# Kernel optimization log

Measured on AMD Instinct MI355X. Metric: run time of the kernel, lower is better.

## Reference

```python
import jax, jax.numpy as jnp
import numpy as np

BATCH, SEQ, IN_DIM, HID = 32, 4096, 256, 256

def setup_inputs() -> dict:
    key = jax.random.key(0)
    ks = jax.random.split(key, 7)
    s_in = 1.0 / np.sqrt(IN_DIM)
    s_h = 1.0 / np.sqrt(HID)
    return {
        "X": jax.random.normal(ks[0], (BATCH, SEQ, IN_DIM), dtype=jnp.float32),
        "Wx_w": jax.random.uniform(ks[1], (HID, IN_DIM), jnp.float32, -s_in, s_in),
        "Wx_b": jax.random.uniform(ks[2], (HID,), jnp.float32, -s_in, s_in),
        "Wh_w": jax.random.uniform(ks[3], (HID, HID), jnp.float32, -s_h, s_h),
        "Wh_b": jax.random.uniform(ks[4], (HID,), jnp.float32, -s_h, s_h),
        "Wy_w": jax.random.uniform(ks[5], (HID, HID), jnp.float32, -s_h, s_h),
        "Wy_b": jax.random.uniform(ks[6], (HID,), jnp.float32, -s_h, s_h),
    }

def reference(X, Wx_w, Wx_b, Wh_w, Wh_b, Wy_w, Wy_b):
    # X: [B, T, D] -> time-major [T, B, D]
    Xt = jnp.transpose(X, (1, 0, 2))
    B = X.shape[0]
    h0 = jnp.zeros((B, Wh_w.shape[0]), dtype=X.dtype)
    # Precompute input projection for all timesteps in one big GEMM
    Xproj = jnp.einsum('tbd,hd->tbh', Xt, Wx_w) + Wx_b  # [T, B, H]

    def step(h, xp):
        h = jnp.tanh(h @ Wh_w.T + Wh_b + xp)   # [B, H]
        y = h @ Wy_w.T + Wy_b                   # [B, H]
        return h, y

    _, Ys = jax.lax.scan(step, h0, Xproj)       # Ys: [T, B, H]
    # torch.cat along dim 0 of per-step [B, H] tensors -> [T*B, H]
    return Ys.reshape(-1, Ys.shape[-1])
```

## Files before the change

kernel.cpp:

```cpp
#include <hip/hip_runtime.h>
#include <cmath>

#define TSEQ 4096
#define NB   32
#define DIM  256

__global__ __launch_bounds__(256) void k1_xproj(
    const float* __restrict__ X, const float* __restrict__ Wx,
    const float* __restrict__ bx, const float* __restrict__ bh,
    float* __restrict__ out)
{
    __shared__ __align__(16) float As[32][68];
    __shared__ __align__(16) float Bs[32][68];
    const int tid = threadIdx.x;
    const int r0 = blockIdx.x * 64;
    const int n0 = blockIdx.y * 64;
    const int tm = tid >> 4, tn = tid & 15;
    const int lr = tid >> 2;
    const int lk = (tid & 3) * 8;

    const int rg = r0 + lr;
    const float* arow = X + ((size_t)(rg & 31) * TSEQ + (size_t)(rg >> 5)) * DIM;
    const float* brow = Wx + (size_t)(n0 + lr) * DIM;

    float acc[4][4] = {};

    for (int k0 = 0; k0 < DIM; k0 += 32) {
        float4 a0 = *(const float4*)(arow + k0 + lk);
        float4 a1 = *(const float4*)(arow + k0 + lk + 4);
        float4 b0 = *(const float4*)(brow + k0 + lk);
        float4 b1 = *(const float4*)(brow + k0 + lk + 4);
        __syncthreads();
        As[lk+0][lr]=a0.x; As[lk+1][lr]=a0.y; As[lk+2][lr]=a0.z; As[lk+3][lr]=a0.w;
        As[lk+4][lr]=a1.x; As[lk+5][lr]=a1.y; As[lk+6][lr]=a1.z; As[lk+7][lr]=a1.w;
        Bs[lk+0][lr]=b0.x; Bs[lk+1][lr]=b0.y; Bs[lk+2][lr]=b0.z; Bs[lk+3][lr]=b0.w;
        Bs[lk+4][lr]=b1.x; Bs[lk+5][lr]=b1.y; Bs[lk+6][lr]=b1.z; Bs[lk+7][lr]=b1.w;
        __syncthreads();
        #pragma unroll
        for (int k = 0; k < 32; ++k) {
            float4 av = *(const float4*)&As[k][4*tm];
            float4 bv = *(const float4*)&Bs[k][4*tn];
            float avv[4] = {av.x, av.y, av.z, av.w};
            float bvv[4] = {bv.x, bv.y, bv.z, bv.w};
            #pragma unroll
            for (int i = 0; i < 4; ++i)
                #pragma unroll
                for (int j = 0; j < 4; ++j)
                    acc[i][j] = fmaf(avv[i], bvv[j], acc[i][j]);
        }
    }

    float4 bxa = *(const float4*)(bx + n0 + 4*tn);
    float4 bha = *(const float4*)(bh + n0 + 4*tn);
    float bias[4] = {bxa.x + bha.x, bxa.y + bha.y, bxa.z + bha.z, bxa.w + bha.w};
    #pragma unroll
    for (int i = 0; i < 4; ++i) {
        size_t r = (size_t)(r0 + 4*tm + i);
        float4 o = make_float4(acc[i][0] + bias[0], acc[i][1] + bias[1],
                               acc[i][2] + bias[2], acc[i][3] + bias[3]);
        *(float4*)(out + r*DIM + n0 + 4*tn) = o;
    }
}

__global__ __launch_bounds__(512, 2) void k2_rnn(
    const float* __restrict__ Wh, float* __restrict__ XH)
{
    const int b = blockIdx.x;
    const int tid = threadIdx.x;
    const int j = tid & 255;
    const int s = tid >> 8;

    __shared__ __align__(16) float hs[256];
    __shared__ __align__(16) float part[256];

    float w[128];
    {
        const float* wb = Wh + (size_t)j * DIM + 128 * s;
        #pragma unroll
        for (int kk = 0; kk < 128; kk += 4) {
            float4 v = *(const float4*)(wb + kk);
            w[kk+0]=v.x; w[kk+1]=v.y; w[kk+2]=v.z; w[kk+3]=v.w;
        }
    }

    if (s == 0) hs[j] = 0.0f;
    float xp_cur = 0.0f;
    if (s == 0) xp_cur = XH[(size_t)b * DIM + j];
    asm volatile("s_waitcnt lgkmcnt(0)\n\ts_barrier" ::: "memory");

    const float* hbase = &hs[128 * s];

    for (int t = 0; t < TSEQ; ++t) {
        const int t1 = (t + 1 < TSEQ) ? (t + 1) : t;
        float xp_nxt = 0.0f;
        if (s == 0) xp_nxt = XH[((size_t)t1 * NB + b) * DIM + j];

        float a0 = 0.f, a1 = 0.f, a2 = 0.f, a3 = 0.f;
        #pragma unroll
        for (int kk = 0; kk < 128; kk += 16) {
            float4 h0 = *(const float4*)(hbase + kk);
            float4 h1 = *(const float4*)(hbase + kk + 4);
            float4 h2 = *(const float4*)(hbase + kk + 8);
            float4 h3 = *(const float4*)(hbase + kk + 12);
            a0 = fmaf(w[kk+ 0], h0.x, a0); a1 = fmaf(w[kk+ 1], h0.y, a1);
            a2 = fmaf(w[kk+ 2], h0.z, a2); a3 = fmaf(w[kk+ 3], h0.w, a3);
            a0 = fmaf(w[kk+ 4], h1.x, a0); a1 = fmaf(w[kk+ 5], h1.y, a1);
            a2 = fmaf(w[kk+ 6], h1.z, a2); a3 = fmaf(w[kk+ 7], h1.w, a3);
            a0 = fmaf(w[kk+ 8], h2.x, a0); a1 = fmaf(w[kk+ 9], h2.y, a1);
            a2 = fmaf(w[kk+10], h2.z, a2); a3 = fmaf(w[kk+11], h2.w, a3);
            a0 = fmaf(w[kk+12], h3.x, a0); a1 = fmaf(w[kk+13], h3.y, a1);
            a2 = fmaf(w[kk+14], h3.z, a2); a3 = fmaf(w[kk+15], h3.w, a3);
        }
        float acc = (a0 + a1) + (a2 + a3);

        if (s) part[j] = acc;
        asm volatile("s_waitcnt lgkmcnt(0)\n\ts_barrier" ::: "memory");

        if (s == 0) {
            float sum = acc + part[j] + xp_cur;
            float e = __builtin_amdgcn_exp2f(sum * 2.8853900817779268f);
            float r = __builtin_amdgcn_rcpf(e + 1.0f);
            float hn = fmaf(-2.0f, r, 1.0f);
            hs[j] = hn;
            XH[((size_t)t * NB + b) * DIM + j] = hn;
        }
        xp_cur = xp_nxt;
        asm volatile("s_waitcnt lgkmcnt(0)\n\ts_barrier" ::: "memory");
    }
}

__global__ __launch_bounds__(256) void k3_y(
    const float* __restrict__ Wy, const float* __restrict__ by,
    float* __restrict__ XH)
{
    __shared__ __align__(16) float As[32][68];
    __shared__ __align__(16) float Bs[32][264];
    const int tid = threadIdx.x;
    const int r0 = blockIdx.x * 64;
    const int tm = tid >> 4, tn = tid & 15;
    const int lr = tid >> 2;
    const int lk = (tid & 3) * 8;

    const float* arow = XH + (size_t)(r0 + lr) * DIM;
    const float* brow = Wy + (size_t)tid * DIM;

    float acc[4][4][4] = {};

    for (int k0 = 0; k0 < DIM; k0 += 32) {
        float4 a0 = *(const float4*)(arow + k0 + lk);
        float4 a1 = *(const float4*)(arow + k0 + lk + 4);
        float4 wv[8];
        #pragma unroll
        for (int i = 0; i < 8; ++i) wv[i] = *(const float4*)(brow + k0 + 4*i);
        __syncthreads();
        As[lk+0][lr]=a0.x; As[lk+1][lr]=a0.y; As[lk+2][lr]=a0.z; As[lk+3][lr]=a0.w;
        As[lk+4][lr]=a1.x; As[lk+5][lr]=a1.y; As[lk+6][lr]=a1.z; As[lk+7][lr]=a1.w;
        #pragma unroll
        for (int i = 0; i < 8; ++i) {
            Bs[4*i+0][tid] = wv[i].x;
            Bs[4*i+1][tid] = wv[i].y;
            Bs[4*i+2][tid] = wv[i].z;
            Bs[4*i+3][tid] = wv[i].w;
        }
        __syncthreads();
        #pragma unroll
        for (int k = 0; k < 32; ++k) {
            float4 av = *(const float4*)&As[k][4*tm];
            float avv[4] = {av.x, av.y, av.z, av.w};
            #pragma unroll
            for (int c = 0; c < 4; ++c) {
                float4 bv = *(const float4*)&Bs[k][64*c + 4*tn];
                #pragma unroll
                for (int i = 0; i < 4; ++i) {
                    acc[i][c][0] = fmaf(avv[i], bv.x, acc[i][c][0]);
                    acc[i][c][1] = fmaf(avv[i], bv.y, acc[i][c][1]);
                    acc[i][c][2] = fmaf(avv[i], bv.z, acc[i][c][2]);
                    acc[i][c][3] = fmaf(avv[i], bv.w, acc[i][c][3]);
                }
            }
        }
    }

    float4 byv[4];
    #pragma unroll
    for (int c = 0; c < 4; ++c) byv[c] = *(const float4*)(by + 64*c + 4*tn);
    #pragma unroll
    for (int i = 0; i < 4; ++i) {
        size_t r = (size_t)(r0 + 4*tm + i);
        #pragma unroll
        for (int c = 0; c < 4; ++c) {
            float4 o = make_float4(acc[i][c][0] + byv[c].x, acc[i][c][1] + byv[c].y,
                                   acc[i][c][2] + byv[c].z, acc[i][c][3] + byv[c].w);
            *(float4*)(XH + r*DIM + 64*c + 4*tn) = o;
        }
    }
}

extern "C" void kernel_launch(void* const* d_in, const int* in_sizes, int n_in,
                              void* d_out, int out_size, void* d_ws, size_t ws_size,
                              hipStream_t stream)
{
    const float* X    = (const float*)d_in[0];
    const float* Wx_w = (const float*)d_in[1];
    const float* Wx_b = (const float*)d_in[2];
    const float* Wh_w = (const float*)d_in[3];
    const float* Wh_b = (const float*)d_in[4];
    const float* Wy_w = (const float*)d_in[5];
    const float* Wy_b = (const float*)d_in[6];
    float* out = (float*)d_out;

    dim3 g1((TSEQ * NB) / 64, DIM / 64);
    k1_xproj<<<g1, 256, 0, stream>>>(X, Wx_w, Wx_b, Wh_b, out);

    k2_rnn<<<NB, 512, 0, stream>>>(Wh_w, out);

    k3_y<<<(TSEQ * NB) / 64, 256, 0, stream>>>(Wy_w, Wy_b, out);
}
```

Baseline: 3.523 ms.

## Use packed FMA in GEMMs and split RNN recurrence over four thread groups

Rewrites the inner loops of both GEMM kernels and the recurrent kernel to use two-wide float vector FMAs, so the compiler can emit packed FP32 FMA instructions. The recurrent kernel now runs 1024 threads per block, splitting the 256-long dot product into four 64-element slices, with three partial-sum buffers reduced by the first group. This shortens the serial per-step dot-product chain that dominates the scan. In exchange there are more waves per barrier and a slightly longer reduction, and the launch-bounds hint of 4 blocks of 1024 threads may be unachievable.

```diff
diff --git a/kernel.cpp b/kernel.cpp
--- a/kernel.cpp
+++ b/kernel.cpp
@@ -4,6 +4,15 @@
 #define TSEQ 4096
 #define NB   32
 #define DIM  256
+
+typedef float f2v __attribute__((ext_vector_type(2)));
+typedef float f4v __attribute__((ext_vector_type(4)));
+
+__device__ __forceinline__ f2v fma2(f2v a, f2v b, f2v c) {
+    return __builtin_elementwise_fma(a, b, c);
+}
+__device__ __forceinline__ f2v lo2(f4v v) { return __builtin_shufflevector(v, v, 0, 1); }
+__device__ __forceinline__ f2v hi2(f4v v) { return __builtin_shufflevector(v, v, 2, 3); }
 
 __global__ __launch_bounds__(256) void k1_xproj(
     const float* __restrict__ X, const float* __restrict__ Wx,
@@ -23,7 +32,7 @@
     const float* arow = X + ((size_t)(rg & 31) * TSEQ + (size_t)(rg >> 5)) * DIM;
     const float* brow = Wx + (size_t)(n0 + lr) * DIM;
 
-    float acc[4][4] = {};
+    f2v acc2[4][2] = {};
 
     for (int k0 = 0; k0 < DIM; k0 += 32) {
         float4 a0 = *(const float4*)(arow + k0 + lk);
@@ -38,15 +47,15 @@
         __syncthreads();
         #pragma unroll
         for (int k = 0; k < 32; ++k) {
-            float4 av = *(const float4*)&As[k][4*tm];
-            float4 bv = *(const float4*)&Bs[k][4*tn];
-            float avv[4] = {av.x, av.y, av.z, av.w};
-            float bvv[4] = {bv.x, bv.y, bv.z, bv.w};
+            f4v av = *(const f4v*)&As[k][4*tm];
+            f4v bv = *(const f4v*)&Bs[k][4*tn];
+            f2v b01 = lo2(bv), b23 = hi2(bv);
             #pragma unroll
-            for (int i = 0; i < 4; ++i)
-                #pragma unroll
-                for (int j = 0; j < 4; ++j)
-                    acc[i][j] = fmaf(avv[i], bvv[j], acc[i][j]);
+            for (int i = 0; i < 4; ++i) {
+                f2v ai = {av[i], av[i]};
+                acc2[i][0] = fma2(ai, b01, acc2[i][0]);
+                acc2[i][1] = fma2(ai, b23, acc2[i][1]);
+            }
         }
     }
 
@@ -56,13 +65,13 @@
     #pragma unroll
     for (int i = 0; i < 4; ++i) {
         size_t r = (size_t)(r0 + 4*tm + i);
-        float4 o = make_float4(acc[i][0] + bias[0], acc[i][1] + bias[1],
-                               acc[i][2] + bias[2], acc[i][3] + bias[3]);
+        float4 o = make_float4(acc2[i][0].x + bias[0], acc2[i][0].y + bias[1],
+                               acc2[i][1].x + bias[2], acc2[i][1].y + bias[3]);
         *(float4*)(out + r*DIM + n0 + 4*tn) = o;
     }
 }
 
-__global__ __launch_bounds__(512, 2) void k2_rnn(
+__global__ __launch_bounds__(1024, 4) void k2_rnn(
     const float* __restrict__ Wh, float* __restrict__ XH)
 {
     const int b = blockIdx.x;
@@ -71,15 +80,16 @@
     const int s = tid >> 8;
 
     __shared__ __align__(16) float hs[256];
-    __shared__ __align__(16) float part[256];
-
-    float w[128];
+    __shared__ __align__(16) float part[3][256];
+
+    f2v w2[32];
     {
-        const float* wb = Wh + (size_t)j * DIM + 128 * s;
-        #pragma unroll
-        for (int kk = 0; kk < 128; kk += 4) {
-            float4 v = *(const float4*)(wb + kk);
-            w[kk+0]=v.x; w[kk+1]=v.y; w[kk+2]=v.z; w[kk+3]=v.w;
+        const float* wb = Wh + (size_t)j * DIM + 64 * s;
+        #pragma unroll
+        for (int kk = 0; kk < 64; kk += 4) {
+            f4v v = *(const f4v*)(wb + kk);
+            w2[kk/2]     = lo2(v);
+            w2[kk/2 + 1] = hi2(v);
         }
     }
 
@@ -88,36 +98,30 @@
     if (s == 0) xp_cur = XH[(size_t)b * DIM + j];
     asm volatile("s_waitcnt lgkmcnt(0)\n\ts_barrier" ::: "memory");
 
-    const float* hbase = &hs[128 * s];
+    const float* hbase = &hs[64 * s];
 
     for (int t = 0; t < TSEQ; ++t) {
         const int t1 = (t + 1 < TSEQ) ? (t + 1) : t;
         float xp_nxt = 0.0f;
         if (s == 0) xp_nxt = XH[((size_t)t1 * NB + b) * DIM + j];
 
-        float a0 = 0.f, a1 = 0.f, a2 = 0.f, a3 = 0.f;
-        #pragma unroll
-        for (int kk = 0; kk < 128; kk += 16) {
-            float4 h0 = *(const float4*)(hbase + kk);
-            float4 h1 = *(const float4*)(hbase + kk + 4);
-            float4 h2 = *(const float4*)(hbase + kk + 8);
-            float4 h3 = *(const float4*)(hbase + kk + 12);
-            a0 = fmaf(w[kk+ 0], h0.x, a0); a1 = fmaf(w[kk+ 1], h0.y, a1);
-            a2 = fmaf(w[kk+ 2], h0.z, a2); a3 = fmaf(w[kk+ 3], h0.w, a3);
-            a0 = fmaf(w[kk+ 4], h1.x, a0); a1 = fmaf(w[kk+ 5], h1.y, a1);
-            a2 = fmaf(w[kk+ 6], h1.z, a2); a3 = fmaf(w[kk+ 7], h1.w, a3);
-            a0 = fmaf(w[kk+ 8], h2.x, a0); a1 = fmaf(w[kk+ 9], h2.y, a1);
-            a2 = fmaf(w[kk+10], h2.z, a2); a3 = fmaf(w[kk+11], h2.w, a3);
-            a0 = fmaf(w[kk+12], h3.x, a0); a1 = fmaf(w[kk+13], h3.y, a1);
-            a2 = fmaf(w[kk+14], h3.z, a2); a3 = fmaf(w[kk+15], h3.w, a3);
-        }
-        float acc = (a0 + a1) + (a2 + a3);
-
-        if (s) part[j] = acc;
+        f2v acc0 = {0.f, 0.f}, acc1 = {0.f, 0.f};
+        #pragma unroll
+        for (int kk = 0; kk < 64; kk += 8) {
+            f4v h0 = *(const f4v*)(hbase + kk);
+            f4v h1 = *(const f4v*)(hbase + kk + 4);
+            acc0 = fma2(w2[kk/2 + 0], lo2(h0), acc0);
+            acc1 = fma2(w2[kk/2 + 1], hi2(h0), acc1);
+            acc0 = fma2(w2[kk/2 + 2], lo2(h1), acc0);
+            acc1 = fma2(w2[kk/2 + 3], hi2(h1), acc1);
+        }
+        float acc = (acc0.x + acc1.x) + (acc0.y + acc1.y);
+
+        if (s) part[s-1][j] = acc;
         asm volatile("s_waitcnt lgkmcnt(0)\n\ts_barrier" ::: "memory");
 
         if (s == 0) {
-            float sum = acc + part[j] + xp_cur;
+            float sum = ((acc + part[0][j]) + (part[1][j] + part[2][j])) + xp_cur;
             float e = __builtin_amdgcn_exp2f(sum * 2.8853900817779268f);
             float r = __builtin_amdgcn_rcpf(e + 1.0f);
             float hn = fmaf(-2.0f, r, 1.0f);
@@ -144,7 +148,7 @@
     const float* arow = XH + (size_t)(r0 + lr) * DIM;
     const float* brow = Wy + (size_t)tid * DIM;
 
-    float acc[4][4][4] = {};
+    f2v acc2[4][4][2] = {};
 
     for (int k0 = 0; k0 < DIM; k0 += 32) {
         float4 a0 = *(const float4*)(arow + k0 + lk);
@@ -165,17 +169,16 @@
         __syncthreads();
         #pragma unroll
         for (int k = 0; k < 32; ++k) {
-            float4 av = *(const float4*)&As[k][4*tm];
-            float avv[4] = {av.x, av.y, av.z, av.w};
+            f4v av = *(const f4v*)&As[k][4*tm];
             #pragma unroll
             for (int c = 0; c < 4; ++c) {
-                float4 bv = *(const float4*)&Bs[k][64*c + 4*tn];
+                f4v bv = *(const f4v*)&Bs[k][64*c + 4*tn];
+                f2v b01 = lo2(bv), b23 = hi2(bv);
                 #pragma unroll
                 for (int i = 0; i < 4; ++i) {
-                    acc[i][c][0] = fmaf(avv[i], bv.x, acc[i][c][0]);
-                    acc[i][c][1] = fmaf(avv[i], bv.y, acc[i][c][1]);
-                    acc[i][c][2] = fmaf(avv[i], bv.z, acc[i][c][2]);
-                    acc[i][c][3] = fmaf(avv[i], bv.w, acc[i][c][3]);
+                    f2v ai = {av[i], av[i]};
+                    acc2[i][c][0] = fma2(ai, b01, acc2[i][c][0]);
+                    acc2[i][c][1] = fma2(ai, b23, acc2[i][c][1]);
                 }
             }
         }
@@ -189,8 +192,8 @@
         size_t r = (size_t)(r0 + 4*tm + i);
         #pragma unroll
         for (int c = 0; c < 4; ++c) {
-            float4 o = make_float4(acc[i][c][0] + byv[c].x, acc[i][c][1] + byv[c].y,
-                                   acc[i][c][2] + byv[c].z, acc[i][c][3] + byv[c].w);
+            float4 o = make_float4(acc2[i][c][0].x + byv[c].x, acc2[i][c][0].y + byv[c].y,
+                                   acc2[i][c][1].x + byv[c].z, acc2[i][c][1].y + byv[c].w);
             *(float4*)(XH + r*DIM + 64*c + 4*tn) = o;
         }
     }
@@ -212,7 +215,7 @@
     dim3 g1((TSEQ * NB) / 64, DIM / 64);
     k1_xproj<<<g1, 256, 0, stream>>>(X, Wx_w, Wx_b, Wh_b, out);
 
-    k2_rnn<<<NB, 512, 0, stream>>>(Wh_w, out);
+    k2_rnn<<<NB, 1024, 0, stream>>>(Wh_w, out);
 
     k3_y<<<(TSEQ * NB) / 64, 256, 0, stream>>>(Wy_w, Wy_b, out);
 }
```

After: 3.711 ms. +5.3%, slower.
